# Performance work log

Hardware: AMD Instinct MI355X
Metric: run time of the kernel (lower is better)

Reference implementation:

```python
import jax, jax.numpy as jnp
import numpy as np

N = 50000      # nodes
E = 800000     # edges (before self-loops)
F_IN = 256
H = 8          # heads layer 1
C = 64         # hidden channels per head
OUT = 40       # classes
NEG_SLOPE = 0.2


def setup_inputs() -> dict:
    key = jax.random.key(0)
    ks = jax.random.split(key, 10)
    sc = 0.05
    return {
        "x": jax.random.normal(ks[0], (N, F_IN), jnp.float32),
        "edge_index": jax.random.randint(ks[1], (2, E), 0, N, dtype=jnp.int64),
        "W1": jax.random.normal(ks[2], (F_IN, H * C), jnp.float32) * sc,
        "a_src1": jax.random.normal(ks[3], (H, C), jnp.float32) * sc,
        "a_dst1": jax.random.normal(ks[4], (H, C), jnp.float32) * sc,
        "b1": jnp.zeros((H * C,), jnp.float32),
        "W2": jax.random.normal(ks[5], (H * C, OUT), jnp.float32) * sc,
        "a_src2": jax.random.normal(ks[6], (1, OUT), jnp.float32) * sc,
        "a_dst2": jax.random.normal(ks[7], (1, OUT), jnp.float32) * sc,
        "b2": jnp.zeros((OUT,), jnp.float32),
    }


def gat_layer(h_in, src, dst, W, a_s, a_d, b, heads, ch, concat, n):
    # h: [n, heads, ch] per-head linear transform
    h = (h_in @ W).reshape(n, heads, ch)
    alpha_s = jnp.sum(h * a_s, axis=-1)   # [n, heads]
    alpha_d = jnp.sum(h * a_d, axis=-1)   # [n, heads]
    # edge-wise raw attention logits [E, heads]
    e = jax.nn.leaky_relu(alpha_s[src] + alpha_d[dst], NEG_SLOPE)
    # segment softmax over incoming edges of each dst node
    m = jax.ops.segment_max(e, dst, num_segments=n)
    w = jnp.exp(e - m[dst])
    s = jax.ops.segment_sum(w, dst, num_segments=n)
    alpha = w / s[dst]                    # [E, heads]
    # scatter-aggregate messages: [n, heads, ch]
    out = jax.ops.segment_sum(h[src] * alpha[:, :, None], dst, num_segments=n)
    out = out.reshape(n, heads * ch) if concat else out.mean(axis=1)
    return out + b


def reference(x, edge_index, W1, a_src1, a_dst1, b1, W2, a_src2, a_dst2, b2):
    # add self-loops (PyG GATConv default); guarantees every dst has >=1 edge
    loop = jnp.arange(N, dtype=edge_index.dtype)
    src = jnp.concatenate([edge_index[0], loop])
    dst = jnp.concatenate([edge_index[1], loop])
    h = gat_layer(x, src, dst, W1, a_src1, a_dst1, b1, H, C, True, N)
    h = jax.nn.relu(h)  # dropout is identity in eval mode
    out = gat_layer(h, src, dst, W2, a_src2, a_dst2, b2, 1, OUT, False, N)
    return jax.nn.log_softmax(out, axis=1)
```

## Files before the change

kernel.cpp:

```cpp
#include <hip/hip_runtime.h>

#define N_NODES 50000
#define N_EDGES 800000
#define F_INK   256
#define HC      512
#define OUT_C   40
#define OUT_P   48
#define NEG     0.2f
#define CAP     64
#define GEMM_NB 782
#define CHUNKS  782
#define PART_SZ 6250
#define SCAT_NB (CHUNKS * 8)

typedef short short8 __attribute__((ext_vector_type(8)));
typedef float f32x4 __attribute__((ext_vector_type(4)));
typedef float f32x2 __attribute__((ext_vector_type(2)));

__device__ __forceinline__ float bf2f(unsigned short u) {
    union { unsigned int i; float f; } v; v.i = ((unsigned int)u) << 16; return v.f;
}
__device__ __forceinline__ unsigned short f2bf(float f) {
    union { float f; unsigned int i; } v; v.f = f;
    unsigned int x = v.i;
    return (unsigned short)((x + 0x7fffu + ((x >> 16) & 1u)) >> 16);
}
__device__ __forceinline__ float bflo(unsigned int u) {
    union { unsigned int i; float f; } v; v.i = u << 16; return v.f;
}
__device__ __forceinline__ float bfhi(unsigned int u) {
    union { unsigned int i; float f; } v; v.i = u & 0xffff0000u; return v.f;
}
__device__ __forceinline__ bool ei_is64(const int* ei) {
    return ei[1] == 0 && ei[3] == 0 && ei[5] == 0;
}
__device__ __forceinline__ float lrelu(float x) { return x > 0.f ? x : NEG * x; }
__device__ __forceinline__ unsigned char f2fp8(float v) {
    return (unsigned char)(__builtin_amdgcn_cvt_pk_fp8_f32(v, v, 0, false) & 0xff);
}
__device__ __forceinline__ float fp82f(unsigned char b) {
    f32x2 p = __builtin_amdgcn_cvt_pk_f32_fp8((int)b, false);
    return p[0];
}

__global__ __launch_bounds__(256) void prep_k(const float* __restrict__ W1, const float* __restrict__ W2,
                       const float* __restrict__ s1, const float* __restrict__ d1, const float* __restrict__ b1,
                       const float* __restrict__ s2, const float* __restrict__ d2, const float* __restrict__ b2,
                       unsigned short* __restrict__ W1p, unsigned short* __restrict__ W2p,
                       unsigned short* __restrict__ s1c, unsigned short* __restrict__ d1c,
                       unsigned short* __restrict__ b1c, unsigned short* __restrict__ s2c,
                       unsigned short* __restrict__ d2c, unsigned short* __restrict__ b2c,
                       int* __restrict__ cnt) {
    int b = blockIdx.x;
    if (b < 512) {
        int t = b * 256 + threadIdx.x;
        int k = t / HC, n = t % HC;
        int s = k >> 5, q = (k >> 3) & 3, j = k & 7;
        W1p[((((s << 2) + q) * HC + n) << 3) + j] = f2bf(W1[k * HC + n]);
    } else if (b < 608) {
        int t = (b - 512) * 256 + threadIdx.x;
        int k = t / OUT_P, n = t % OUT_P;
        int s = k >> 5, q = (k >> 3) & 3, j = k & 7;
        unsigned short v = (n < OUT_C) ? f2bf(W2[k * OUT_C + n]) : (unsigned short)0;
        W2p[((((s << 2) + q) * OUT_P + n) << 3) + j] = v;
    } else if (b == 608) {
        int t = threadIdx.x;
        for (int j = t; j < 512; j += 256) {
            s1c[j] = f2bf(s1[j]); d1c[j] = f2bf(d1[j]); b1c[j] = f2bf(b1[j]);
        }
        if (t < OUT_C) { s2c[t] = f2bf(s2[t]); d2c[t] = f2bf(d2[t]); b2c[t] = f2bf(b2[t]); }
    } else {
        int i = (b - 609) * 256 + threadIdx.x;
        if (i < N_NODES) cnt[i * 16] = 0;
    }
}

__global__ __launch_bounds__(256) void gemm1_k(const float* __restrict__ x,
                                               const unsigned short* __restrict__ Wp,
                                               const unsigned short* __restrict__ a_s,
                                               const unsigned short* __restrict__ a_d,
                                               unsigned char* __restrict__ h1f8,
                                               float* __restrict__ as1, float* __restrict__ ad1,
                                               const int* __restrict__ ei,
                                               int* __restrict__ cnt, int* __restrict__ srcs) {
    __shared__ unsigned short xs[64 * 264];
    int tid = threadIdx.x;
    if (blockIdx.x >= GEMM_NB) {
        int sb = blockIdx.x - GEMM_NB;
        int part = blockIdx.x & 7;
        int chunk = sb >> 3;
        int lo = part * PART_SZ;
        bool is64 = ei_is64(ei);
        int e0 = chunk * 1024 + (tid << 2);
        int s[4], d[4];
        bool vld[4];
        if (chunk < CHUNKS - 1) {
            if (is64) {
                int4 a0 = *reinterpret_cast<const int4*>(ei + 2 * e0);
                int4 a1 = *reinterpret_cast<const int4*>(ei + 2 * e0 + 4);
                int4 c0 = *reinterpret_cast<const int4*>(ei + 2 * N_EDGES + 2 * e0);
                int4 c1 = *reinterpret_cast<const int4*>(ei + 2 * N_EDGES + 2 * e0 + 4);
                s[0] = a0.x; s[1] = a0.z; s[2] = a1.x; s[3] = a1.z;
                d[0] = c0.x; d[1] = c0.z; d[2] = c1.x; d[3] = c1.z;
            } else {
                int4 a0 = *reinterpret_cast<const int4*>(ei + e0);
                int4 c0 = *reinterpret_cast<const int4*>(ei + N_EDGES + e0);
                s[0] = a0.x; s[1] = a0.y; s[2] = a0.z; s[3] = a0.w;
                d[0] = c0.x; d[1] = c0.y; d[2] = c0.z; d[3] = c0.w;
            }
            vld[0] = vld[1] = vld[2] = vld[3] = true;
        } else {
#pragma unroll
            for (int j = 0; j < 4; j++) {
                int e = e0 + j;
                vld[j] = e < N_EDGES;
                int ec = vld[j] ? e : 0;
                s[j] = is64 ? ei[2 * ec] : ei[ec];
                d[j] = is64 ? ei[2 * N_EDGES + 2 * ec] : ei[N_EDGES + ec];
            }
        }
#pragma unroll
        for (int j = 0; j < 4; j++) {
            int dj = d[j];
            if (vld[j] && dj >= lo && dj < lo + PART_SZ) {
                int pos = atomicAdd(&cnt[dj * 16], 1);
                if (pos < CAP) srcs[(size_t)dj * CAP + pos] = s[j];
            }
        }
        return;
    }
    int bm = blockIdx.x;
    int row0 = bm * 64;
#pragma unroll
    for (int it = 0; it < 16; it++) {
        int j = tid + it * 256;
        int r = j >> 6;
        int c = (j & 63) << 2;
        int rr = row0 + r; rr = rr < N_NODES ? rr : N_NODES - 1;
        float4 f = *reinterpret_cast<const float4*>(x + (size_t)rr * F_INK + c);
        unsigned int lo = (unsigned int)f2bf(f.x) | ((unsigned int)f2bf(f.y) << 16);
        unsigned int hi = (unsigned int)f2bf(f.z) | ((unsigned int)f2bf(f.w) << 16);
        *reinterpret_cast<uint2*>(&xs[r * 264 + c]) = make_uint2(lo, hi);
    }
    __syncthreads();
    int w = tid >> 6, lane = tid & 63;
    int q = lane >> 4, l16 = lane & 15;
    short8 a[8];
#pragma unroll
    for (int s = 0; s < 8; s++)
        a[s] = *reinterpret_cast<const short8*>(&xs[(w * 16 + l16) * 264 + s * 32 + q * 8]);
    int orow = row0 + w * 16 + q * 4;
#pragma unroll
    for (int bn = 0; bn < 8; bn++) {
        f32x4 acc[4];
#pragma unroll
        for (int t = 0; t < 4; t++) acc[t] = (f32x4){0.f, 0.f, 0.f, 0.f};
#pragma unroll
        for (int s = 0; s < 8; s++) {
#pragma unroll
            for (int t = 0; t < 4; t++) {
                int col = bn * 64 + t * 16 + l16;
                short8 b = *reinterpret_cast<const short8*>(Wp + ((((s << 2) + q) * HC + col) << 3));
                acc[t] = __builtin_amdgcn_mfma_f32_16x16x32_bf16(a[s], b, acc[t], 0, 0, 0);
            }
        }
        float sa0 = 0.f, sa1 = 0.f, sa2 = 0.f, sa3 = 0.f;
        float da0 = 0.f, da1 = 0.f, da2 = 0.f, da3 = 0.f;
#pragma unroll
        for (int t = 0; t < 4; t++) {
            int col = bn * 64 + t * 16 + l16;
            float asc = bf2f(a_s[col]);
            float adc = bf2f(a_d[col]);
            float v0 = acc[t][0], v1 = acc[t][1], v2 = acc[t][2], v3 = acc[t][3];
            sa0 += v0 * asc; da0 += v0 * adc;
            sa1 += v1 * asc; da1 += v1 * adc;
            sa2 += v2 * asc; da2 += v2 * adc;
            sa3 += v3 * asc; da3 += v3 * adc;
            if (orow + 3 < N_NODES) {
                h1f8[(size_t)(orow + 0) * HC + col] = f2fp8(v0);
                h1f8[(size_t)(orow + 1) * HC + col] = f2fp8(v1);
                h1f8[(size_t)(orow + 2) * HC + col] = f2fp8(v2);
                h1f8[(size_t)(orow + 3) * HC + col] = f2fp8(v3);
            } else {
                if (orow + 0 < N_NODES) h1f8[(size_t)(orow + 0) * HC + col] = f2fp8(v0);
                if (orow + 1 < N_NODES) h1f8[(size_t)(orow + 1) * HC + col] = f2fp8(v1);
                if (orow + 2 < N_NODES) h1f8[(size_t)(orow + 2) * HC + col] = f2fp8(v2);
                if (orow + 3 < N_NODES) h1f8[(size_t)(orow + 3) * HC + col] = f2fp8(v3);
            }
        }
#pragma unroll
        for (int m = 1; m < 16; m <<= 1) {
            sa0 += __shfl_xor(sa0, m, 64); sa1 += __shfl_xor(sa1, m, 64);
            sa2 += __shfl_xor(sa2, m, 64); sa3 += __shfl_xor(sa3, m, 64);
            da0 += __shfl_xor(da0, m, 64); da1 += __shfl_xor(da1, m, 64);
            da2 += __shfl_xor(da2, m, 64); da3 += __shfl_xor(da3, m, 64);
        }
        if (l16 < 4) {
            int rr = orow + l16;
            float sav = (l16 == 0) ? sa0 : (l16 == 1) ? sa1 : (l16 == 2) ? sa2 : sa3;
            float dav = (l16 == 0) ? da0 : (l16 == 1) ? da1 : (l16 == 2) ? da2 : da3;
            if (rr < N_NODES) { as1[rr * 8 + bn] = sav; ad1[rr * 8 + bn] = dav; }
        }
    }
}

#define ACCPK(u, wgt)                                                        \
    {                                                                        \
        f32x2 p0 = __builtin_amdgcn_cvt_pk_f32_fp8((int)(u).x, false);       \
        f32x2 p1 = __builtin_amdgcn_cvt_pk_f32_fp8((int)(u).x, true);        \
        f32x2 p2 = __builtin_amdgcn_cvt_pk_f32_fp8((int)(u).y, false);       \
        f32x2 p3 = __builtin_amdgcn_cvt_pk_f32_fp8((int)(u).y, true);        \
        f32x2 wv = {(wgt), (wgt)};                                           \
        acc01 += wv * p0; acc23 += wv * p1;                                  \
        acc45 += wv * p2; acc67 += wv * p3;                                  \
    }

__global__ __launch_bounds__(256) void agg1_k(const unsigned char* __restrict__ h1f8,
                                              const float* __restrict__ as1,
                                              const float* __restrict__ ad1,
                                              const int* __restrict__ cnt,
                                              const int* __restrict__ srcs,
                                              const unsigned short* __restrict__ b1,
                                              const unsigned short* __restrict__ W2p,
                                              const unsigned short* __restrict__ a_s2,
                                              const unsigned short* __restrict__ a_d2,
                                              unsigned char* __restrict__ h2f8) {
    __shared__ unsigned short rows[16 * 520];
    __shared__ float sAs[16], sAd[16];
    __shared__ int ctr;
    int tid = threadIdx.x;
    if (tid < 16) { sAs[tid] = 0.f; sAd[tid] = 0.f; }
    if (tid == 0) ctr = 0;
    __syncthreads();
    int w = tid >> 6, lane = tid & 63;
    int h = lane >> 3;
    int base = blockIdx.x * 16;
    uint4 ub = *(reinterpret_cast<const uint4*>(b1) + lane);
    for (;;) {
        int rl = 0;
        if (lane == 0) rl = atomicAdd(&ctr, 1);
        rl = __shfl(rl, 0, 64);
        if (rl >= 16) break;
        int wid = base + rl;
        float adv = ad1[wid * 8 + h];
        f32x2 acc01 = {0.f, 0.f}, acc23 = {0.f, 0.f}, acc45 = {0.f, 0.f}, acc67 = {0.f, 0.f};
        float sumw = 0.f;
        int e = wid * CAP, e1 = e + cnt[wid * 16];
        for (; e + 12 <= e1; e += 12) {
            int s[12];
            float A[12];
            uint2 u[12];
#pragma unroll
            for (int j = 0; j < 12; j++) s[j] = srcs[e + j];
#pragma unroll
            for (int j = 0; j < 12; j++) A[j] = as1[s[j] * 8 + h];
#pragma unroll
            for (int j = 0; j < 12; j++)
                u[j] = reinterpret_cast<const uint2*>(h1f8 + (size_t)s[j] * HC)[lane];
#pragma unroll
            for (int j = 0; j < 12; j++) {
                float wj = __expf(lrelu(A[j] + adv));
                sumw += wj;
                ACCPK(u[j], wj)
            }
        }
        for (; e + 4 <= e1; e += 4) {
            int s[4];
            float A[4];
            uint2 u[4];
#pragma unroll
            for (int j = 0; j < 4; j++) s[j] = srcs[e + j];
#pragma unroll
            for (int j = 0; j < 4; j++) A[j] = as1[s[j] * 8 + h];
#pragma unroll
            for (int j = 0; j < 4; j++)
                u[j] = reinterpret_cast<const uint2*>(h1f8 + (size_t)s[j] * HC)[lane];
#pragma unroll
            for (int j = 0; j < 4; j++) {
                float wj = __expf(lrelu(A[j] + adv));
                sumw += wj;
                ACCPK(u[j], wj)
            }
        }
        for (; e < e1; e++) {
            int s0 = srcs[e];
            float wj = __expf(lrelu(as1[s0 * 8 + h] + adv));
            uint2 u0 = reinterpret_cast<const uint2*>(h1f8 + (size_t)s0 * HC)[lane];
            sumw += wj;
            ACCPK(u0, wj)
        }
        {
            float wj = __expf(lrelu(as1[wid * 8 + h] + adv));
            uint2 u0 = reinterpret_cast<const uint2*>(h1f8 + (size_t)wid * HC)[lane];
            sumw += wj;
            ACCPK(u0, wj)
        }
        float inv = 1.f / sumw;
        float o0 = fmaxf(acc01[0] * inv + bflo(ub.x), 0.f);
        float o1 = fmaxf(acc01[1] * inv + bfhi(ub.x), 0.f);
        float o2 = fmaxf(acc23[0] * inv + bflo(ub.y), 0.f);
        float o3 = fmaxf(acc23[1] * inv + bfhi(ub.y), 0.f);
        float o4 = fmaxf(acc45[0] * inv + bflo(ub.z), 0.f);
        float o5 = fmaxf(acc45[1] * inv + bfhi(ub.z), 0.f);
        float o6 = fmaxf(acc67[0] * inv + bflo(ub.w), 0.f);
        float o7 = fmaxf(acc67[1] * inv + bfhi(ub.w), 0.f);
        uint4 r;
        r.x = (unsigned int)f2bf(o0) | ((unsigned int)f2bf(o1) << 16);
        r.y = (unsigned int)f2bf(o2) | ((unsigned int)f2bf(o3) << 16);
        r.z = (unsigned int)f2bf(o4) | ((unsigned int)f2bf(o5) << 16);
        r.w = (unsigned int)f2bf(o6) | ((unsigned int)f2bf(o7) << 16);
        *reinterpret_cast<uint4*>(&rows[rl * 520 + lane * 8]) = r;
    }
    __syncthreads();
    if (w < 3) {
        int q = lane >> 4, l16 = lane & 15;
        int col = w * 16 + l16;
        f32x4 acc = (f32x4){0.f, 0.f, 0.f, 0.f};
#pragma unroll
        for (int s = 0; s < HC / 32; s++) {
            short8 a = *reinterpret_cast<const short8*>(&rows[l16 * 520 + s * 32 + q * 8]);
            short8 b = *reinterpret_cast<const short8*>(W2p + ((((s << 2) + q) * OUT_P + col) << 3));
            acc = __builtin_amdgcn_mfma_f32_16x16x32_bf16(a, b, acc, 0, 0, 0);
        }
        float sa0 = 0.f, sa1 = 0.f, sa2 = 0.f, sa3 = 0.f;
        float da0 = 0.f, da1 = 0.f, da2 = 0.f, da3 = 0.f;
        if (col < OUT_C) {
            float asc = bf2f(a_s2[col]);
            float adc = bf2f(a_d2[col]);
            sa0 = acc[0] * asc; da0 = acc[0] * adc;
            sa1 = acc[1] * asc; da1 = acc[1] * adc;
            sa2 = acc[2] * asc; da2 = acc[2] * adc;
            sa3 = acc[3] * asc; da3 = acc[3] * adc;
#pragma unroll
            for (int r = 0; r < 4; r++)
                h2f8[(size_t)(base + q * 4 + r) * 64 + col] = f2fp8(acc[r]);
        }
#pragma unroll
        for (int m = 1; m < 16; m <<= 1) {
            sa0 += __shfl_xor(sa0, m, 64); sa1 += __shfl_xor(sa1, m, 64);
            sa2 += __shfl_xor(sa2, m, 64); sa3 += __shfl_xor(sa3, m, 64);
            da0 += __shfl_xor(da0, m, 64); da1 += __shfl_xor(da1, m, 64);
            da2 += __shfl_xor(da2, m, 64); da3 += __shfl_xor(da3, m, 64);
        }
        if (l16 < 4) {
            int rr = q * 4 + l16;
            float sav = (l16 == 0) ? sa0 : (l16 == 1) ? sa1 : (l16 == 2) ? sa2 : sa3;
            float dav = (l16 == 0) ? da0 : (l16 == 1) ? da1 : (l16 == 2) ? da2 : da3;
            atomicAdd(&sAs[rr], sav);
            atomicAdd(&sAd[rr], dav);
        }
    }
    __syncthreads();
    if (tid < 16) {
        unsigned char* r = h2f8 + (size_t)(base + tid) * 64;
        *reinterpret_cast<float*>(r + 40) = sAs[tid];
        *reinterpret_cast<float*>(r + 44) = sAd[tid];
    }
}

__global__ __launch_bounds__(256) void agg2_k(const unsigned char* __restrict__ h2f8,
                                              const int* __restrict__ cnt,
                                              const int* __restrict__ srcs,
                                              const unsigned short* __restrict__ b2,
                                              float* __restrict__ outp) {
    int wid = blockIdx.x * 4 + (threadIdx.x >> 6);
    if (wid >= N_NODES) return;
    int lane = threadIdx.x & 63;
    bool act = lane < OUT_C;
    int lclamp = act ? lane : 0;
    const unsigned char* rd = h2f8 + (size_t)wid * 64;
    float adv = *reinterpret_cast<const float*>(rd + 44);
    float acc, sumw;
    {
        float w0 = __expf(lrelu(*reinterpret_cast<const float*>(rd + 40) + adv));
        sumw = w0;
        acc = w0 * fp82f(rd[lclamp]);
    }
    int e = wid * CAP, e1 = e + cnt[wid * 16];
    for (; e + 4 <= e1; e += 4) {
        int s0 = srcs[e], s1 = srcs[e + 1], s2 = srcs[e + 2], s3 = srcs[e + 3];
        const unsigned char* r0 = h2f8 + (size_t)s0 * 64;
        const unsigned char* r1 = h2f8 + (size_t)s1 * 64;
        const unsigned char* r2 = h2f8 + (size_t)s2 * 64;
        const unsigned char* r3 = h2f8 + (size_t)s3 * 64;
        float A0 = *reinterpret_cast<const float*>(r0 + 40);
        float A1 = *reinterpret_cast<const float*>(r1 + 40);
        float A2 = *reinterpret_cast<const float*>(r2 + 40);
        float A3 = *reinterpret_cast<const float*>(r3 + 40);
        unsigned char c0 = r0[lclamp];
        unsigned char c1 = r1[lclamp];
        unsigned char c2 = r2[lclamp];
        unsigned char c3 = r3[lclamp];
        float w0 = __expf(lrelu(A0 + adv));
        float w1 = __expf(lrelu(A1 + adv));
        float w2 = __expf(lrelu(A2 + adv));
        float w3 = __expf(lrelu(A3 + adv));
        sumw += (w0 + w1) + (w2 + w3);
        acc += w0 * fp82f(c0) + w1 * fp82f(c1) + w2 * fp82f(c2) + w3 * fp82f(c3);
    }
    for (; e < e1; e++) {
        int s0 = srcs[e];
        const unsigned char* r0 = h2f8 + (size_t)s0 * 64;
        float w0 = __expf(lrelu(*reinterpret_cast<const float*>(r0 + 40) + adv));
        sumw += w0;
        acc += w0 * fp82f(r0[lclamp]);
    }
    float o = acc / sumw + bf2f(b2[lclamp]);
    float mval = act ? o : -1e30f;
#pragma unroll
    for (int m = 32; m >= 1; m >>= 1) mval = fmaxf(mval, __shfl_xor(mval, m, 64));
    float ex = act ? __expf(o - mval) : 0.f;
#pragma unroll
    for (int m = 32; m >= 1; m >>= 1) ex += __shfl_xor(ex, m, 64);
    float res = o - mval - __logf(ex);
    if (act) outp[(size_t)wid * OUT_C + lane] = res;
}

extern "C" void kernel_launch(void* const* d_in, const int* in_sizes, int n_in,
                              void* d_out, int out_size, void* d_ws, size_t ws_size,
                              hipStream_t stream) {
    const float* x      = (const float*)d_in[0];
    const int*   ei     = (const int*)d_in[1];
    const float* W1     = (const float*)d_in[2];
    const float* as1raw = (const float*)d_in[3];
    const float* ad1raw = (const float*)d_in[4];
    const float* b1raw  = (const float*)d_in[5];
    const float* W2     = (const float*)d_in[6];
    const float* as2raw = (const float*)d_in[7];
    const float* ad2raw = (const float*)d_in[8];
    const float* b2raw  = (const float*)d_in[9];
    float* out = (float*)d_out;

    char* p = (char*)d_ws;
    auto alloc = [&](size_t bytes) -> char* {
        char* r = p;
        p += (bytes + 255) & ~(size_t)255;
        return r;
    };
    unsigned short* s1c  = (unsigned short*)alloc(512 * 2);
    unsigned short* d1c  = (unsigned short*)alloc(512 * 2);
    unsigned short* b1c  = (unsigned short*)alloc(512 * 2);
    unsigned short* s2c  = (unsigned short*)alloc(OUT_C * 2);
    unsigned short* d2c  = (unsigned short*)alloc(OUT_C * 2);
    unsigned short* b2c  = (unsigned short*)alloc(OUT_C * 2);
    unsigned char*  h1f8 = (unsigned char*)alloc((size_t)N_NODES * HC);
    unsigned char*  h2f8 = (unsigned char*)alloc((size_t)N_NODES * 64);
    float* as1  = (float*)alloc((size_t)N_NODES * 8 * 4);
    float* ad1  = (float*)alloc((size_t)N_NODES * 8 * 4);
    int* cnt    = (int*)alloc((size_t)N_NODES * 64);
    int* srcs   = (int*)alloc((size_t)N_NODES * CAP * 4);
    unsigned short* W1p = (unsigned short*)alloc((size_t)F_INK * HC * 2);
    unsigned short* W2p = (unsigned short*)alloc((size_t)HC * OUT_P * 2);
    (void)ws_size; (void)in_sizes; (void)n_in; (void)out_size;

    const int NB = (N_NODES + 255) / 256;

    prep_k<<<609 + NB, 256, 0, stream>>>(W1, W2, as1raw, ad1raw, b1raw, as2raw, ad2raw, b2raw,
                                         W1p, W2p, s1c, d1c, b1c, s2c, d2c, b2c, cnt);
    gemm1_k<<<GEMM_NB + SCAT_NB, 256, 0, stream>>>(x, W1p, s1c, d1c, h1f8, as1, ad1,
                                                   ei, cnt, srcs);
    agg1_k<<<N_NODES / 16, 256, 0, stream>>>(h1f8, as1, ad1, cnt, srcs, b1c,
                                             W2p, s2c, d2c, h2f8);
    agg2_k<<<(N_NODES + 3) / 4, 256, 0, stream>>>(h2f8, cnt, srcs, b2c, out);
}
```

Measured before the change: 288.9 us.

## Split agg1 wave into two half-waves processing alternate edges with 16-byte loads

The layer-1 aggregation kernel now splits each wavefront into two 32-lane halves. Each half handles alternate incoming edges and each lane loads 16 fp8 channels (uint4) instead of 8. The two halves' partial sums are combined with a cross-half shuffle, the self-loop is folded into the first iteration, and degree is clamped to CAP in both aggregation kernels. This aims to double memory-level parallelism and widen each gather, at the cost of twice the accumulator registers, extra shuffles, and masked tail handling.

Measured after the change: 283.5 us. No clear change (-1.9%).

```diff
diff --git a/kernel.cpp b/kernel.cpp
--- a/kernel.cpp
+++ b/kernel.cpp
@@ -34,7 +34,7 @@
 __device__ __forceinline__ bool ei_is64(const int* ei) {
     return ei[1] == 0 && ei[3] == 0 && ei[5] == 0;
 }
-__device__ __forceinline__ float lrelu(float x) { return x > 0.f ? x : NEG * x; }
+__device__ __forceinline__ float lrelu(float x) { return fmaxf(x, NEG * x); }
 __device__ __forceinline__ unsigned char f2fp8(float v) {
     return (unsigned char)(__builtin_amdgcn_cvt_pk_fp8_f32(v, v, 0, false) & 0xff);
 }
@@ -204,15 +204,19 @@
     }
 }
 
-#define ACCPK(u, wgt)                                                        \
-    {                                                                        \
-        f32x2 p0 = __builtin_amdgcn_cvt_pk_f32_fp8((int)(u).x, false);       \
-        f32x2 p1 = __builtin_amdgcn_cvt_pk_f32_fp8((int)(u).x, true);        \
-        f32x2 p2 = __builtin_amdgcn_cvt_pk_f32_fp8((int)(u).y, false);       \
-        f32x2 p3 = __builtin_amdgcn_cvt_pk_f32_fp8((int)(u).y, true);        \
-        f32x2 wv = {(wgt), (wgt)};                                           \
-        acc01 += wv * p0; acc23 += wv * p1;                                  \
-        acc45 += wv * p2; acc67 += wv * p3;                                  \
+#define ACC16(u, wgt)                                                              \
+    {                                                                              \
+        f32x2 q0 = __builtin_amdgcn_cvt_pk_f32_fp8((int)(u).x, false);             \
+        f32x2 q1 = __builtin_amdgcn_cvt_pk_f32_fp8((int)(u).x, true);              \
+        f32x2 q2 = __builtin_amdgcn_cvt_pk_f32_fp8((int)(u).y, false);             \
+        f32x2 q3 = __builtin_amdgcn_cvt_pk_f32_fp8((int)(u).y, true);              \
+        f32x2 q4 = __builtin_amdgcn_cvt_pk_f32_fp8((int)(u).z, false);             \
+        f32x2 q5 = __builtin_amdgcn_cvt_pk_f32_fp8((int)(u).z, true);              \
+        f32x2 q6 = __builtin_amdgcn_cvt_pk_f32_fp8((int)(u).w, false);             \
+        f32x2 q7 = __builtin_amdgcn_cvt_pk_f32_fp8((int)(u).w, true);              \
+        f32x2 wv = {(wgt), (wgt)};                                                 \
+        ac[0] += wv * q0; ac[1] += wv * q1; ac[2] += wv * q2; ac[3] += wv * q3;    \
+        ac[4] += wv * q4; ac[5] += wv * q5; ac[6] += wv * q6; ac[7] += wv * q7;    \
     }
 
 __global__ __launch_bounds__(256) void agg1_k(const unsigned char* __restrict__ h1f8,
@@ -233,9 +237,11 @@
     if (tid == 0) ctr = 0;
     __syncthreads();
     int w = tid >> 6, lane = tid & 63;
-    int h = lane >> 3;
+    int half = lane >> 5, li = lane & 31;
+    int h = li >> 2;
     int base = blockIdx.x * 16;
-    uint4 ub = *(reinterpret_cast<const uint4*>(b1) + lane);
+    uint4 ub0 = reinterpret_cast<const uint4*>(b1)[li * 2 + 0];
+    uint4 ub1 = reinterpret_cast<const uint4*>(b1)[li * 2 + 1];
     for (;;) {
         int rl = 0;
         if (lane == 0) rl = atomicAdd(&ctr, 1);
@@ -243,73 +249,89 @@
         if (rl >= 16) break;
         int wid = base + rl;
         float adv = ad1[wid * 8 + h];
-        f32x2 acc01 = {0.f, 0.f}, acc23 = {0.f, 0.f}, acc45 = {0.f, 0.f}, acc67 = {0.f, 0.f};
+        f32x2 ac[8];
+#pragma unroll
+        for (int k = 0; k < 8; k++) ac[k] = (f32x2){0.f, 0.f};
         float sumw = 0.f;
-        int e = wid * CAP, e1 = e + cnt[wid * 16];
-        for (; e + 12 <= e1; e += 12) {
-            int s[12];
-            float A[12];
-            uint2 u[12];
-#pragma unroll
-            for (int j = 0; j < 12; j++) s[j] = srcs[e + j];
-#pragma unroll
-            for (int j = 0; j < 12; j++) A[j] = as1[s[j] * 8 + h];
-#pragma unroll
-            for (int j = 0; j < 12; j++)
-                u[j] = reinterpret_cast<const uint2*>(h1f8 + (size_t)s[j] * HC)[lane];
-#pragma unroll
-            for (int j = 0; j < 12; j++) {
-                float wj = __expf(lrelu(A[j] + adv));
-                sumw += wj;
-                ACCPK(u[j], wj)
-            }
-        }
-        for (; e + 4 <= e1; e += 4) {
-            int s[4];
-            float A[4];
-            uint2 u[4];
-#pragma unroll
-            for (int j = 0; j < 4; j++) s[j] = srcs[e + j];
+        int deg = cnt[wid * 16]; deg = deg < CAP ? deg : CAP;
+        int e0 = wid * CAP;
+        {
+            int s = half ? (deg > 0 ? srcs[e0] : wid) : wid;
+            float A = as1[s * 8 + h];
+            uint4 u = reinterpret_cast<const uint4*>(h1f8 + (size_t)s * HC)[li];
+            float wj = (half && deg == 0) ? 0.f : __expf(lrelu(A + adv));
+            sumw += wj;
+            ACC16(u, wj)
+        }
+        int v = 1;
+        for (; v + 8 <= deg; v += 8) {
+            int s[4]; float A[4]; uint4 u[4];
+#pragma unroll
+            for (int j = 0; j < 4; j++) s[j] = srcs[e0 + v + 2 * j + half];
 #pragma unroll
             for (int j = 0; j < 4; j++) A[j] = as1[s[j] * 8 + h];
 #pragma unroll
             for (int j = 0; j < 4; j++)
-                u[j] = reinterpret_cast<const uint2*>(h1f8 + (size_t)s[j] * HC)[lane];
+                u[j] = reinterpret_cast<const uint4*>(h1f8 + (size_t)s[j] * HC)[li];
 #pragma unroll
             for (int j = 0; j < 4; j++) {
                 float wj = __expf(lrelu(A[j] + adv));
                 sumw += wj;
-                ACCPK(u[j], wj)
-            }
-        }
-        for (; e < e1; e++) {
-            int s0 = srcs[e];
-            float wj = __expf(lrelu(as1[s0 * 8 + h] + adv));
-            uint2 u0 = reinterpret_cast<const uint2*>(h1f8 + (size_t)s0 * HC)[lane];
+                ACC16(u[j], wj)
+            }
+        }
+        for (; v + 4 <= deg; v += 4) {
+            int s[2]; float A[2]; uint4 u[2];
+#pragma unroll
+            for (int j = 0; j < 2; j++) s[j] = srcs[e0 + v + 2 * j + half];
+#pragma unroll
+            for (int j = 0; j < 2; j++) A[j] = as1[s[j] * 8 + h];
+#pragma unroll
+            for (int j = 0; j < 2; j++)
+                u[j] = reinterpret_cast<const uint4*>(h1f8 + (size_t)s[j] * HC)[li];
+#pragma unroll
+            for (int j = 0; j < 2; j++) {
+                float wj = __expf(lrelu(A[j] + adv));
+                sumw += wj;
+                ACC16(u[j], wj)
+            }
+        }
+        for (; v < deg; v += 2) {
+            int vv = v + half;
+            bool ok = vv < deg;
+            int s = ok ? srcs[e0 + vv] : wid;
+            float A = as1[s * 8 + h];
+            uint4 u = reinterpret_cast<const uint4*>(h1f8 + (size_t)s * HC)[li];
+            float wj = ok ? __expf(lrelu(A + adv)) : 0.f;
             sumw += wj;
-            ACCPK(u0, wj)
-        }
-        {
-            float wj = __expf(lrelu(as1[wid * 8 + h] + adv));
-            uint2 u0 = reinterpret_cast<const uint2*>(h1f8 + (size_t)wid * HC)[lane];
-            sumw += wj;
-            ACCPK(u0, wj)
+            ACC16(u, wj)
+        }
+        sumw += __shfl_xor(sumw, 32, 64);
+#pragma unroll
+        for (int k = 0; k < 8; k++) {
+            ac[k][0] += __shfl_xor(ac[k][0], 32, 64);
+            ac[k][1] += __shfl_xor(ac[k][1], 32, 64);
         }
         float inv = 1.f / sumw;
-        float o0 = fmaxf(acc01[0] * inv + bflo(ub.x), 0.f);
-        float o1 = fmaxf(acc01[1] * inv + bfhi(ub.x), 0.f);
-        float o2 = fmaxf(acc23[0] * inv + bflo(ub.y), 0.f);
-        float o3 = fmaxf(acc23[1] * inv + bfhi(ub.y), 0.f);
-        float o4 = fmaxf(acc45[0] * inv + bflo(ub.z), 0.f);
-        float o5 = fmaxf(acc45[1] * inv + bfhi(ub.z), 0.f);
-        float o6 = fmaxf(acc67[0] * inv + bflo(ub.w), 0.f);
-        float o7 = fmaxf(acc67[1] * inv + bfhi(ub.w), 0.f);
+        f32x2 n0 = half ? ac[4] : ac[0];
+        f32x2 n1 = half ? ac[5] : ac[1];
+        f32x2 n2 = half ? ac[6] : ac[2];
+        f32x2 n3 = half ? ac[7] : ac[3];
+        uint4 ubh = half ? ub1 : ub0;
+        float o0 = fmaxf(n0[0] * inv + bflo(ubh.x), 0.f);
+        float o1 = fmaxf(n0[1] * inv + bfhi(ubh.x), 0.f);
+        float o2 = fmaxf(n1[0] * inv + bflo(ubh.y), 0.f);
+        float o3 = fmaxf(n1[1] * inv + bfhi(ubh.y), 0.f);
+        float o4 = fmaxf(n2[0] * inv + bflo(ubh.z), 0.f);
+        float o5 = fmaxf(n2[1] * inv + bfhi(ubh.z), 0.f);
+        float o6 = fmaxf(n3[0] * inv + bflo(ubh.w), 0.f);
+        float o7 = fmaxf(n3[1] * inv + bfhi(ubh.w), 0.f);
         uint4 r;
         r.x = (unsigned int)f2bf(o0) | ((unsigned int)f2bf(o1) << 16);
         r.y = (unsigned int)f2bf(o2) | ((unsigned int)f2bf(o3) << 16);
         r.z = (unsigned int)f2bf(o4) | ((unsigned int)f2bf(o5) << 16);
         r.w = (unsigned int)f2bf(o6) | ((unsigned int)f2bf(o7) << 16);
-        *reinterpret_cast<uint4*>(&rows[rl * 520 + lane * 8]) = r;
+        *reinterpret_cast<uint4*>(&rows[rl * 520 + li * 16 + half * 8]) = r;
     }
     __syncthreads();
     if (w < 3) {
@@ -376,7 +398,8 @@
         sumw = w0;
         acc = w0 * fp82f(rd[lclamp]);
     }
-    int e = wid * CAP, e1 = e + cnt[wid * 16];
+    int deg = cnt[wid * 16]; deg = deg < CAP ? deg : CAP;
+    int e = wid * CAP, e1 = e + deg;
     for (; e + 4 <= e1; e += 4) {
         int s0 = srcs[e], s1 = srcs[e + 1], s2 = srcs[e + 2], s3 = srcs[e + 3];
         const unsigned char* r0 = h2f8 + (size_t)s0 * 64;
```
